# Performance work log

Hardware: AMD Instinct MI355X
Metric: run time of the kernel (lower is better)

Reference implementation:

```python
import jax, jax.numpy as jnp
import numpy as np


def setup_inputs() -> dict:
    key = jax.random.key(0)
    kq, kk, kv = jax.random.split(key, 3)
    B, L, H, D = 2, 4096, 8, 64
    queries = jax.random.normal(kq, (B, L, H, D), dtype=jnp.float32)
    keys = jax.random.normal(kk, (B, L, H, D), dtype=jnp.float32)
    values = jax.random.normal(kv, (B, L, H, D), dtype=jnp.float32)
    return {"queries": queries, "keys": keys, "values": values}


def reference(queries, keys, values):
    # queries/keys/values: [B, L, H, D]
    d_model = queries.shape[-1]
    scale = 1.0 / jnp.sqrt(jnp.asarray(d_model, dtype=queries.dtype))
    # scores: [B, H, Lq, Lk]
    scores = jnp.einsum('blhd,bshd->bhls', queries, keys)
    # dropout is identity in eval mode / for deterministic reference
    A = jax.nn.softmax(scale * scores, axis=-1)
    # output: [B, Lq, H, D]
    V = jnp.einsum('bhls,bshd->blhd', A, values)
    return V
```

## Files before the change

kernel.cpp:

```cpp
#include <hip/hip_runtime.h>

#define Bn 2
#define Ln 4096
#define Hn 8
#define Dn 64
#define NMEGA 32
#define BH_STRIDE 262144

typedef float    f32x4  __attribute__((ext_vector_type(4)));
typedef float    f32x16 __attribute__((ext_vector_type(16)));
typedef _Float16 f16x2  __attribute__((ext_vector_type(2)));
typedef _Float16 f16x8  __attribute__((ext_vector_type(8)));
typedef unsigned int u32;
typedef u32 u32x2 __attribute__((ext_vector_type(2)));
typedef u32 u32x4 __attribute__((ext_vector_type(4)));

static __device__ __forceinline__ void gld16(const void* g, void* l){
    __builtin_amdgcn_global_load_lds(
        (const __attribute__((address_space(1))) unsigned int*)g,
        (__attribute__((address_space(3))) unsigned int*)l, 16, 0, 0);
}

static __device__ __forceinline__ u32 pkf16(float a, float b){
    auto h = __builtin_amdgcn_cvt_pkrtz(a, b);
    return __builtin_bit_cast(u32, h);
}

static __device__ __forceinline__ u32x2 swp(u32 a, u32 b){
    auto r = __builtin_amdgcn_permlane32_swap(a, b, false, false);
    return __builtin_bit_cast(u32x2, r);
}

__global__ __launch_bounds__(256)
void kvprep(const float* __restrict__ Kg, const float* __restrict__ Vg,
            _Float16* __restrict__ kp, _Float16* __restrict__ vp){
    __shared__ float tV[64*65];
    const int t = blockIdx.x, bh = blockIdx.y, b = bh>>3, h = bh&7;
    const int tid = threadIdx.x;
#pragma unroll
    for(int i=0;i<4;++i){
        int idx = tid + i*256;
        int k = idx >> 4, d4 = (idx & 15)*4;
        float4 v = *(const float4*)(Vg + (((size_t)b*Ln + t*64 + k)*Hn + h)*Dn + d4);
        tV[k*65+d4+0]=v.x; tV[k*65+d4+1]=v.y;
        tV[k*65+d4+2]=v.z; tV[k*65+d4+3]=v.w;
    }
#pragma unroll
    for(int i=0;i<2;++i){
        int u = tid + i*256;
        int lane = u & 63, unit = u >> 6;
        int g = unit >> 2, cc = unit & 3;
        const float* src = Kg + (((size_t)b*Ln + t*64 + g*32 + (lane&31))*Hn + h)*Dn
                         + cc*16 + (lane>>5)*8;
        float4 a = *(const float4*)src;
        float4 c4 = *(const float4*)(src + 4);
        f16x8 o;
        o[0]=(_Float16)a.x;  o[1]=(_Float16)a.y;  o[2]=(_Float16)a.z;  o[3]=(_Float16)a.w;
        o[4]=(_Float16)c4.x; o[5]=(_Float16)c4.y; o[6]=(_Float16)c4.z; o[7]=(_Float16)c4.w;
        *(f16x8*)(kp + (size_t)bh*BH_STRIDE + (size_t)t*4096 + (size_t)u*8) = o;
    }
    __syncthreads();
#pragma unroll
    for(int i=0;i<2;++i){
        int u = tid + i*256;
        int lane = u & 63, unit = u >> 6;
        int g = unit >> 2, kh = (unit >> 1) & 1, dt = unit & 1;
        int krow = g*32 + kh*16 + (lane>>5)*8;
        int d = dt*32 + (lane&31);
        f16x8 o;
#pragma unroll
        for(int j=0;j<8;++j) o[j] = (_Float16)tV[(krow+j)*65 + d];
        *(f16x8*)(vp + (size_t)bh*BH_STRIDE + (size_t)t*4096 + (size_t)u*8) = o;
    }
}

static __device__ __forceinline__ f32x16 qk4(const f16x8 kf[4], const f16x8 qf[4]){
    f32x16 s;
#pragma unroll
    for(int r=0;r<16;++r) s[r]=0.f;
    s = __builtin_amdgcn_mfma_f32_32x32x16_f16(kf[0], qf[0], s, 0,0,0);
    s = __builtin_amdgcn_mfma_f32_32x32x16_f16(kf[1], qf[1], s, 0,0,0);
    s = __builtin_amdgcn_mfma_f32_32x32x16_f16(kf[2], qf[2], s, 0,0,0);
    s = __builtin_amdgcn_mfma_f32_32x32x16_f16(kf[3], qf[3], s, 0,0,0);
    return s;
}

static __device__ __forceinline__ void finish_pv(const f32x16& S, float& lac,
                                                 f32x16& o0, f32x16& o1,
                                                 const f16x8 vf[4]){
    f32x16 p;
#pragma unroll
    for(int r=0;r<16;++r) p[r] = __builtin_amdgcn_exp2f(S[r]);
    u32 A0 = pkf16(p[0],p[1]),   A1 = pkf16(p[2],p[3]);
    u32 B0 = pkf16(p[4],p[5]),   B1 = pkf16(p[6],p[7]);
    u32 C0 = pkf16(p[8],p[9]),   C1 = pkf16(p[10],p[11]);
    u32 D0 = pkf16(p[12],p[13]), D1 = pkf16(p[14],p[15]);
    u32x2 r0 = swp(A0,B0), r1 = swp(A1,B1);
    u32x2 r2 = swp(C0,D0), r3 = swp(C1,D1);
    u32x4 w0 = {r0.x, r1.x, r0.y, r1.y};
    u32x4 w1 = {r2.x, r3.x, r2.y, r3.y};
    f16x8 pa0 = __builtin_bit_cast(f16x8, w0);
    f16x8 pa1 = __builtin_bit_cast(f16x8, w1);
    const f16x2 ones = {(_Float16)1.0f, (_Float16)1.0f};
#pragma unroll
    for(int j=0;j<4;++j){
        f16x2 c0 = {pa0[2*j], pa0[2*j+1]};
        f16x2 c1 = {pa1[2*j], pa1[2*j+1]};
        lac = __builtin_amdgcn_fdot2(c0, ones, lac, false);
        lac = __builtin_amdgcn_fdot2(c1, ones, lac, false);
    }
    o0 = __builtin_amdgcn_mfma_f32_32x32x16_f16(pa0, vf[0], o0, 0,0,0);
    o0 = __builtin_amdgcn_mfma_f32_32x32x16_f16(pa1, vf[2], o0, 0,0,0);
    o1 = __builtin_amdgcn_mfma_f32_32x32x16_f16(pa0, vf[1], o1, 0,0,0);
    o1 = __builtin_amdgcn_mfma_f32_32x32x16_f16(pa1, vf[3], o1, 0,0,0);
}

__global__ __launch_bounds__(256,2)
void attn_fwd(const float* __restrict__ Qg, float* __restrict__ Og,
              const _Float16* __restrict__ kp, const _Float16* __restrict__ vp){
    __shared__ __align__(16) _Float16 sKV[4][8192];

    const int tid  = threadIdx.x;
    const int lane = tid & 63, wv = tid >> 6;
    const int qh = wv & 1, kh2 = wv >> 1;
    const int l31 = lane & 31, hi = lane >> 5;
    const int bh = blockIdx.x, b = bh>>3, h = bh&7;
    const int q0 = blockIdx.y*128 + qh*64;

    const float c = 0.125f * 1.4426950408889634f;

    f16x8 qf[2][4];
#pragma unroll
    for(int qt=0;qt<2;++qt){
        const float* qrow = Qg + (((size_t)b*Ln + q0 + qt*32 + l31)*Hn + h)*Dn;
#pragma unroll
        for(int cc=0;cc<4;++cc){
            const float* p4 = qrow + cc*16 + hi*8;
            float4 x = *(const float4*)p4;
            float4 y = *(const float4*)(p4+4);
            f16x8 f;
            f[0]=(_Float16)(x.x*c); f[1]=(_Float16)(x.y*c);
            f[2]=(_Float16)(x.z*c); f[3]=(_Float16)(x.w*c);
            f[4]=(_Float16)(y.x*c); f[5]=(_Float16)(y.y*c);
            f[6]=(_Float16)(y.z*c); f[7]=(_Float16)(y.w*c);
            qf[qt][cc]=f;
        }
    }

    f32x16 o[2][2];
    float lac[2] = {0.f, 0.f};
#pragma unroll
    for(int qt=0;qt<2;++qt)
#pragma unroll
        for(int dt=0;dt<2;++dt)
#pragma unroll
            for(int r=0;r<16;++r) o[qt][dt][r]=0.f;

    const _Float16* kg = kp + (size_t)bh*BH_STRIDE;
    const _Float16* vg = vp + (size_t)bh*BH_STRIDE;

    const int kbyte = kh2*8192 + lane*16;

#pragma unroll
    for(int i=0;i<4;++i){
        int u = i*256 + tid;
        gld16(kg + (size_t)u*8, &sKV[0][(size_t)u*8]);
        gld16(vg + (size_t)u*8, &sKV[2][(size_t)u*8]);
    }

    for(int T=0; T<NMEGA; ++T){
        __syncthreads();
        const int cur = T & 1;
        if(T+1 < NMEGA){
            const int nxt = cur ^ 1;
            const _Float16* kgn = kg + (size_t)(T+1)*8192;
            const _Float16* vgn = vg + (size_t)(T+1)*8192;
#pragma unroll
            for(int i=0;i<4;++i){
                int u = i*256 + tid;
                gld16(kgn + (size_t)u*8, &sKV[nxt][(size_t)u*8]);
                gld16(vgn + (size_t)u*8, &sKV[2+nxt][(size_t)u*8]);
            }
        }

        const char* Kb = (const char*)&sKV[cur][0];
        const char* Vb = (const char*)&sKV[2+cur][0];

        f16x8 kf0[4], vf0[4];
#pragma unroll
        for(int cc=0;cc<4;++cc)
            kf0[cc] = *(const f16x8*)(Kb + ((0*4+cc)<<10) + kbyte);
#pragma unroll
        for(int j=0;j<4;++j)
            vf0[j] = *(const f16x8*)(Vb + ((0*4+j)<<10) + kbyte);

        f32x16 S0 = qk4(kf0, qf[0]);
        f32x16 S1 = qk4(kf0, qf[1]);

        f16x8 kf1[4], vf1[4];
#pragma unroll
        for(int cc=0;cc<4;++cc)
            kf1[cc] = *(const f16x8*)(Kb + ((1*4+cc)<<10) + kbyte);
#pragma unroll
        for(int j=0;j<4;++j)
            vf1[j] = *(const f16x8*)(Vb + ((1*4+j)<<10) + kbyte);

        finish_pv(S0, lac[0], o[0][0], o[0][1], vf0);
        f32x16 S0b = qk4(kf1, qf[0]);
        finish_pv(S1, lac[1], o[1][0], o[1][1], vf0);
        f32x16 S1b = qk4(kf1, qf[1]);
        finish_pv(S0b, lac[0], o[0][0], o[0][1], vf1);
        finish_pv(S1b, lac[1], o[1][0], o[1][1], vf1);
    }

    float lred[2];
#pragma unroll
    for(int qt=0;qt<2;++qt)
        lred[qt] = lac[qt] + __shfl_xor(lac[qt], 32, 64);

    __syncthreads();
    float* xo = (float*)&sKV[0][0];
    float* xl = xo + 128*68;
    if(kh2){
#pragma unroll
        for(int qt=0;qt<2;++qt){
#pragma unroll
            for(int dt=0;dt<2;++dt)
#pragma unroll
                for(int r=0;r<16;++r){
                    int qr = (r&3) + 8*(r>>2) + 4*hi;
                    xo[(qh*64 + qt*32 + qr)*68 + dt*32 + l31] = o[qt][dt][r];
                }
            if(hi==0) xl[qh*64 + qt*32 + l31] = lred[qt];
        }
    }
    __syncthreads();
    if(!kh2){
#pragma unroll
        for(int qt=0;qt<2;++qt){
            float inv = 1.0f/(lred[qt] + xl[qh*64 + qt*32 + l31]);
            float* ob = Og + (((size_t)b*Ln + q0 + qt*32)*Hn + h)*Dn;
#pragma unroll
            for(int r=0;r<16;++r){
                int qr = (r&3) + 8*(r>>2) + 4*hi;
                float invr = __shfl(inv, qr, 64);
#pragma unroll
                for(int dt=0;dt<2;++dt){
                    float val = o[qt][dt][r] + xo[(qh*64 + qt*32 + qr)*68 + dt*32 + l31];
                    ob[(size_t)qr*Hn*Dn + dt*32 + l31] = val*invr;
                }
            }
        }
    }
}

extern "C" void kernel_launch(void* const* d_in, const int* in_sizes, int n_in,
                              void* d_out, int out_size, void* d_ws, size_t ws_size,
                              hipStream_t stream) {
    const float* Q = (const float*)d_in[0];
    const float* K = (const float*)d_in[1];
    const float* V = (const float*)d_in[2];
    float* O = (float*)d_out;

    _Float16* kp = (_Float16*)d_ws;
    _Float16* vp = (_Float16*)((char*)d_ws + (8u<<20));

    kvprep<<<dim3(64, 16), dim3(256), 0, stream>>>(K, V, kp, vp);
    attn_fwd<<<dim3(16, 32), dim3(256), 0, stream>>>(Q, O, kp, vp);
}
```

Measured before the change: 163.1 us.

## Software-pipeline QK scores of the second subtile into the next iteration

The main loop is restructured so the QK^T scores for the second key subtile are computed at the end of one iteration and consumed by softmax/PV at the start of the next. A prologue handles the first mega-tile and an epilogue finishes the last carried scores. A sched_barrier keeps the current QK MFMAs ahead of the carried PV work, so matrix math overlaps the exp/softmax work. The cost is extra live registers for the carried scores and V fragments, which could lower occupancy or cause spills.

```diff
diff --git a/kernel.cpp b/kernel.cpp
--- a/kernel.cpp
+++ b/kernel.cpp
@@ -168,7 +168,38 @@
         gld16(vg + (size_t)u*8, &sKV[2][(size_t)u*8]);
     }
 
-    for(int T=0; T<NMEGA; ++T){
+    f32x16 pS0, pS1;
+    f16x8  pvf[4];
+
+    {
+        __syncthreads();
+#pragma unroll
+        for(int i=0;i<4;++i){
+            int u = i*256 + tid;
+            gld16(kg + 8192 + (size_t)u*8, &sKV[1][(size_t)u*8]);
+            gld16(vg + 8192 + (size_t)u*8, &sKV[3][(size_t)u*8]);
+        }
+        const char* Kb = (const char*)&sKV[0][0];
+        const char* Vb = (const char*)&sKV[2][0];
+        f16x8 kf0[4], vf0[4];
+#pragma unroll
+        for(int cc=0;cc<4;++cc) kf0[cc] = *(const f16x8*)(Kb + (cc<<10) + kbyte);
+#pragma unroll
+        for(int j=0;j<4;++j)    vf0[j]  = *(const f16x8*)(Vb + (j<<10) + kbyte);
+        f32x16 S0 = qk4(kf0, qf[0]);
+        f32x16 S1 = qk4(kf0, qf[1]);
+        f16x8 kf1[4];
+#pragma unroll
+        for(int cc=0;cc<4;++cc) kf1[cc] = *(const f16x8*)(Kb + ((4+cc)<<10) + kbyte);
+#pragma unroll
+        for(int j=0;j<4;++j)    pvf[j]  = *(const f16x8*)(Vb + ((4+j)<<10) + kbyte);
+        finish_pv(S0, lac[0], o[0][0], o[0][1], vf0);
+        finish_pv(S1, lac[1], o[1][0], o[1][1], vf0);
+        pS0 = qk4(kf1, qf[0]);
+        pS1 = qk4(kf1, qf[1]);
+    }
+
+    for(int T=1; T<NMEGA; ++T){
         __syncthreads();
         const int cur = T & 1;
         if(T+1 < NMEGA){
@@ -182,36 +213,32 @@
                 gld16(vgn + (size_t)u*8, &sKV[2+nxt][(size_t)u*8]);
             }
         }
-
         const char* Kb = (const char*)&sKV[cur][0];
         const char* Vb = (const char*)&sKV[2+cur][0];
 
         f16x8 kf0[4], vf0[4];
 #pragma unroll
-        for(int cc=0;cc<4;++cc)
-            kf0[cc] = *(const f16x8*)(Kb + ((0*4+cc)<<10) + kbyte);
-#pragma unroll
-        for(int j=0;j<4;++j)
-            vf0[j] = *(const f16x8*)(Vb + ((0*4+j)<<10) + kbyte);
-
+        for(int cc=0;cc<4;++cc) kf0[cc] = *(const f16x8*)(Kb + (cc<<10) + kbyte);
+#pragma unroll
+        for(int j=0;j<4;++j)    vf0[j]  = *(const f16x8*)(Vb + (j<<10) + kbyte);
         f32x16 S0 = qk4(kf0, qf[0]);
         f32x16 S1 = qk4(kf0, qf[1]);
-
-        f16x8 kf1[4], vf1[4];
-#pragma unroll
-        for(int cc=0;cc<4;++cc)
-            kf1[cc] = *(const f16x8*)(Kb + ((1*4+cc)<<10) + kbyte);
-#pragma unroll
-        for(int j=0;j<4;++j)
-            vf1[j] = *(const f16x8*)(Vb + ((1*4+j)<<10) + kbyte);
-
+        __builtin_amdgcn_sched_barrier(0);
+        finish_pv(pS0, lac[0], o[0][0], o[0][1], pvf);
+        finish_pv(pS1, lac[1], o[1][0], o[1][1], pvf);
+        f16x8 kf1[4];
+#pragma unroll
+        for(int cc=0;cc<4;++cc) kf1[cc] = *(const f16x8*)(Kb + ((4+cc)<<10) + kbyte);
+#pragma unroll
+        for(int j=0;j<4;++j)    pvf[j]  = *(const f16x8*)(Vb + ((4+j)<<10) + kbyte);
         finish_pv(S0, lac[0], o[0][0], o[0][1], vf0);
-        f32x16 S0b = qk4(kf1, qf[0]);
         finish_pv(S1, lac[1], o[1][0], o[1][1], vf0);
-        f32x16 S1b = qk4(kf1, qf[1]);
-        finish_pv(S0b, lac[0], o[0][0], o[0][1], vf1);
-        finish_pv(S1b, lac[1], o[1][0], o[1][1], vf1);
-    }
+        pS0 = qk4(kf1, qf[0]);
+        pS1 = qk4(kf1, qf[1]);
+    }
+
+    finish_pv(pS0, lac[0], o[0][0], o[0][1], pvf);
+    finish_pv(pS1, lac[1], o[1][0], o[1][1], pvf);
 
     float lred[2];
 #pragma unroll
```

After: 168.7 us. 1.03x slower.

## Load K/V fragments directly from global memory instead of LDS double buffer

Applied to the files above, without the earlier changes.

Drops the LDS double-buffered K/V staging through global_load_lds and the per-tile block barriers. Each wave now reads its pre-swizzled f16 K/V fragments straight from global memory into registers, and LDS is kept only for the final cross-wave reduction. Launch bounds are raised to 4 blocks per CU to hide global latency with more occupancy. The cost is more L2/global traffic, since waves sharing a block no longer share staged tiles, and possible register pressure from the higher occupancy target.

```diff
diff --git a/kernel.cpp b/kernel.cpp
--- a/kernel.cpp
+++ b/kernel.cpp
@@ -14,12 +14,6 @@
 typedef unsigned int u32;
 typedef u32 u32x2 __attribute__((ext_vector_type(2)));
 typedef u32 u32x4 __attribute__((ext_vector_type(4)));
-
-static __device__ __forceinline__ void gld16(const void* g, void* l){
-    __builtin_amdgcn_global_load_lds(
-        (const __attribute__((address_space(1))) unsigned int*)g,
-        (__attribute__((address_space(3))) unsigned int*)l, 16, 0, 0);
-}
 
 static __device__ __forceinline__ u32 pkf16(float a, float b){
     auto h = __builtin_amdgcn_cvt_pkrtz(a, b);
@@ -115,10 +109,10 @@
     o1 = __builtin_amdgcn_mfma_f32_32x32x16_f16(pa1, vf[3], o1, 0,0,0);
 }
 
-__global__ __launch_bounds__(256,2)
+__global__ __launch_bounds__(256,4)
 void attn_fwd(const float* __restrict__ Qg, float* __restrict__ Og,
               const _Float16* __restrict__ kp, const _Float16* __restrict__ vp){
-    __shared__ __align__(16) _Float16 sKV[4][8192];
+    __shared__ __align__(16) float xo[128*68 + 128];
 
     const int tid  = threadIdx.x;
     const int lane = tid & 63, wv = tid >> 6;
@@ -156,54 +150,27 @@
 #pragma unroll
             for(int r=0;r<16;++r) o[qt][dt][r]=0.f;
 
-    const _Float16* kg = kp + (size_t)bh*BH_STRIDE;
-    const _Float16* vg = vp + (size_t)bh*BH_STRIDE;
-
-    const int kbyte = kh2*8192 + lane*16;
-
-#pragma unroll
-    for(int i=0;i<4;++i){
-        int u = i*256 + tid;
-        gld16(kg + (size_t)u*8, &sKV[0][(size_t)u*8]);
-        gld16(vg + (size_t)u*8, &sKV[2][(size_t)u*8]);
-    }
+    const char* kgc = (const char*)(kp + (size_t)bh*BH_STRIDE) + kh2*8192 + lane*16;
+    const char* vgc = (const char*)(vp + (size_t)bh*BH_STRIDE) + kh2*8192 + lane*16;
 
     for(int T=0; T<NMEGA; ++T){
-        __syncthreads();
-        const int cur = T & 1;
-        if(T+1 < NMEGA){
-            const int nxt = cur ^ 1;
-            const _Float16* kgn = kg + (size_t)(T+1)*8192;
-            const _Float16* vgn = vg + (size_t)(T+1)*8192;
-#pragma unroll
-            for(int i=0;i<4;++i){
-                int u = i*256 + tid;
-                gld16(kgn + (size_t)u*8, &sKV[nxt][(size_t)u*8]);
-                gld16(vgn + (size_t)u*8, &sKV[2+nxt][(size_t)u*8]);
-            }
-        }
-
-        const char* Kb = (const char*)&sKV[cur][0];
-        const char* Vb = (const char*)&sKV[2+cur][0];
+        const char* Kb = kgc + (size_t)T*16384;
+        const char* Vb = vgc + (size_t)T*16384;
 
         f16x8 kf0[4], vf0[4];
 #pragma unroll
-        for(int cc=0;cc<4;++cc)
-            kf0[cc] = *(const f16x8*)(Kb + ((0*4+cc)<<10) + kbyte);
-#pragma unroll
-        for(int j=0;j<4;++j)
-            vf0[j] = *(const f16x8*)(Vb + ((0*4+j)<<10) + kbyte);
+        for(int cc=0;cc<4;++cc) kf0[cc] = *(const f16x8*)(Kb + (cc<<10));
+#pragma unroll
+        for(int j=0;j<4;++j)    vf0[j]  = *(const f16x8*)(Vb + (j<<10));
 
         f32x16 S0 = qk4(kf0, qf[0]);
         f32x16 S1 = qk4(kf0, qf[1]);
 
         f16x8 kf1[4], vf1[4];
 #pragma unroll
-        for(int cc=0;cc<4;++cc)
-            kf1[cc] = *(const f16x8*)(Kb + ((1*4+cc)<<10) + kbyte);
-#pragma unroll
-        for(int j=0;j<4;++j)
-            vf1[j] = *(const f16x8*)(Vb + ((1*4+j)<<10) + kbyte);
+        for(int cc=0;cc<4;++cc) kf1[cc] = *(const f16x8*)(Kb + ((4+cc)<<10));
+#pragma unroll
+        for(int j=0;j<4;++j)    vf1[j]  = *(const f16x8*)(Vb + ((4+j)<<10));
 
         finish_pv(S0, lac[0], o[0][0], o[0][1], vf0);
         f32x16 S0b = qk4(kf1, qf[0]);
@@ -218,8 +185,6 @@
     for(int qt=0;qt<2;++qt)
         lred[qt] = lac[qt] + __shfl_xor(lac[qt], 32, 64);
 
-    __syncthreads();
-    float* xo = (float*)&sKV[0][0];
     float* xl = xo + 128*68;
     if(kh2){
 #pragma unroll
```

New measurement: 460.3 us. 2.82x slower.
